# Optimization experiments

Hardware: AMD Instinct MI355X
Metric: run time of the kernel (lower is better)

## Reference

```python
import jax, jax.numpy as jnp
import numpy as np

B, N, D_IN = 32, 4096, 768
D_SLOT, K = 256, 8
D_SHAPE, D_TEX = 128, 128
NUM_ITERS = 3
EPS = 1e-8
LN_EPS = 1e-5


def _ln(x, g, b):
    m = jnp.mean(x, axis=-1, keepdims=True)
    v = jnp.mean((x - m) ** 2, axis=-1, keepdims=True)
    return (x - m) * jax.lax.rsqrt(v + LN_EPS) * g + b


def setup_inputs() -> dict:
    key = jax.random.key(0)
    ks = jax.random.split(key, 20)
    s = lambda fan_in: 1.0 / np.sqrt(fan_in)
    d = {}
    d['features'] = jax.random.normal(ks[0], (B, N, D_IN), dtype=jnp.float32)
    # slot init MLP: d_input -> 2*d_slot -> K*d_slot
    d['Wi1'] = jax.random.uniform(ks[1], (D_IN, 2 * D_SLOT), minval=-s(D_IN), maxval=s(D_IN))
    d['bi1'] = jnp.zeros((2 * D_SLOT,), jnp.float32)
    d['Wi2'] = jax.random.uniform(ks[2], (2 * D_SLOT, K * D_SLOT), minval=-s(2 * D_SLOT), maxval=s(2 * D_SLOT))
    d['bi2'] = jnp.zeros((K * D_SLOT,), jnp.float32)
    # input_proj Linear + LayerNorm
    d['Wp'] = jax.random.uniform(ks[3], (D_IN, D_SLOT), minval=-s(D_IN), maxval=s(D_IN))
    d['bp'] = jnp.zeros((D_SLOT,), jnp.float32)
    d['ln_in_g'] = jnp.ones((D_SLOT,), jnp.float32)
    d['ln_in_b'] = jnp.zeros((D_SLOT,), jnp.float32)
    # attention projections (no bias)
    d['Wqs'] = jax.random.uniform(ks[4], (D_SHAPE, D_SHAPE), minval=-s(D_SHAPE), maxval=s(D_SHAPE))
    d['Wks'] = jax.random.uniform(ks[5], (D_SHAPE, D_SHAPE), minval=-s(D_SHAPE), maxval=s(D_SHAPE))
    d['Wqt'] = jax.random.uniform(ks[6], (D_TEX, D_TEX), minval=-s(D_TEX), maxval=s(D_TEX))
    d['Wkt'] = jax.random.uniform(ks[7], (D_TEX, D_TEX), minval=-s(D_TEX), maxval=s(D_TEX))
    # GRUCell (PyTorch layout, gate order r,z,n), stored as [in, 3*hidden]
    d['W_ih'] = jax.random.uniform(ks[8], (D_SLOT, 3 * D_SLOT), minval=-s(D_SLOT), maxval=s(D_SLOT))
    d['W_hh'] = jax.random.uniform(ks[9], (D_SLOT, 3 * D_SLOT), minval=-s(D_SLOT), maxval=s(D_SLOT))
    d['b_ih'] = jax.random.uniform(ks[10], (3 * D_SLOT,), minval=-s(D_SLOT), maxval=s(D_SLOT))
    d['b_hh'] = jax.random.uniform(ks[11], (3 * D_SLOT,), minval=-s(D_SLOT), maxval=s(D_SLOT))
    # slot LayerNorm + MLP
    d['ln_g'] = jnp.ones((D_SLOT,), jnp.float32)
    d['ln_b'] = jnp.zeros((D_SLOT,), jnp.float32)
    d['Wm1'] = jax.random.uniform(ks[12], (D_SLOT, 2 * D_SLOT), minval=-s(D_SLOT), maxval=s(D_SLOT))
    d['bm1'] = jnp.zeros((2 * D_SLOT,), jnp.float32)
    d['Wm2'] = jax.random.uniform(ks[13], (2 * D_SLOT, D_SLOT), minval=-s(2 * D_SLOT), maxval=s(2 * D_SLOT))
    d['bm2'] = jnp.zeros((D_SLOT,), jnp.float32)
    return d


def _gru(x, h, W_ih, W_hh, b_ih, b_hh):
    gx = x @ W_ih + b_ih  # [M, 3H]
    gh = h @ W_hh + b_hh
    xr, xz, xn = jnp.split(gx, 3, axis=-1)
    hr, hz, hn = jnp.split(gh, 3, axis=-1)
    r = jax.nn.sigmoid(xr + hr)
    z = jax.nn.sigmoid(xz + hz)
    n = jnp.tanh(xn + r * hn)
    return (1.0 - z) * n + z * h


def reference(features, Wi1, bi1, Wi2, bi2, Wp, bp, ln_in_g, ln_in_b,
              Wqs, Wks, Wqt, Wkt, W_ih, W_hh, b_ih, b_hh,
              ln_g, ln_b, Wm1, bm1, Wm2, bm2):
    gelu = lambda x: jax.nn.gelu(x, approximate=False)
    Bsz = features.shape[0]
    # input projection + LN: [B, N, D_SLOT]
    inputs = _ln(features @ Wp + bp, ln_in_g, ln_in_b)
    # probabilistic slot init (eval mode: deterministic branch only)
    feat_pool = jnp.mean(features, axis=1)  # [B, D_IN]
    slots = (gelu(feat_pool @ Wi1 + bi1) @ Wi2 + bi2).reshape(Bsz, K, D_SLOT)
    inp_s = inputs[:, :, :D_SHAPE]
    inp_t = inputs[:, :, D_SHAPE:]
    k_s = inp_s @ Wks  # [B, N, Ds]
    k_t = inp_t @ Wkt
    scale_s = D_SHAPE ** -0.5
    scale_t = D_TEX ** -0.5
    attn = None
    for _ in range(NUM_ITERS):
        q_s = slots[:, :, :D_SHAPE] @ Wqs  # [B, K, Ds]
        q_t = slots[:, :, D_SHAPE:] @ Wqt
        attn_shape = jnp.einsum('bkd,bnd->bkn', q_s, k_s) * scale_s
        attn_tex = jnp.einsum('bkd,bnd->bkn', q_t, k_t) * scale_t
        logits = 0.7 * attn_shape + 0.3 * attn_tex  # [B, K, N]
        attn = jax.nn.softmax(logits, axis=1)  # softmax over slots
        attn_normed = attn / (jnp.sum(attn, axis=-1, keepdims=True) + EPS)
        updates = jnp.einsum('bkn,bnd->bkd', attn_normed, inputs)
        h = _gru(updates.reshape(Bsz * K, D_SLOT), slots.reshape(Bsz * K, D_SLOT),
                 W_ih, W_hh, b_ih, b_hh).reshape(Bsz, K, D_SLOT)
        sn = _ln(h, ln_g, ln_b)
        slots = h + (gelu(sn @ Wm1 + bm1) @ Wm2 + bm2)
    return slots, attn, slots[:, :, :D_SHAPE], slots[:, :, D_SHAPE:]
```

## Files before the change

### kernel.cpp

```cpp
#include <hip/hip_runtime.h>
#include <math.h>

#define NB 32
#define NN 4096
#define DIN 768
#define DS 256
#define KS 8
#define MROWS (NB*NN)

typedef short s8v __attribute__((ext_vector_type(8)));
typedef float f4v __attribute__((ext_vector_type(4)));

__device__ __forceinline__ short f2bf(float f) {
    unsigned u = __builtin_bit_cast(unsigned, f);
    u = (u + 0x7FFFu + ((u >> 16) & 1u)) >> 16;
    return (short)u;
}
__device__ __forceinline__ float bf2f(short s) {
    unsigned u = ((unsigned)(unsigned short)s) << 16;
    return __builtin_bit_cast(float, u);
}
__device__ __forceinline__ float gelu_exact(float x) {
    return 0.5f * x * (1.0f + erff(x * 0.70710678118654752f));
}

__global__ __launch_bounds__(256) void prep_weights(const float* Wp, const float* Wks,
                                                    const float* Wkt, short* Wp_sw, short* Wk_sw) {
    int t = blockIdx.x * 256 + threadIdx.x;
    if (t < 24 * 16 * 64) {
        int s = t / (16 * 64), nt = (t / 64) % 16, l = t % 64;
        int q = l >> 4, m = l & 15;
        #pragma unroll
        for (int j = 0; j < 8; ++j)
            Wp_sw[t * 8 + j] = f2bf(Wp[(s * 32 + q * 8 + j) * 256 + nt * 16 + m]);
    } else if (t < 24 * 16 * 64 + 2 * 4 * 8 * 64) {
        int t2 = t - 24 * 16 * 64;
        int half = t2 / (4 * 8 * 64);
        int r = t2 % (4 * 8 * 64);
        int s = r / (8 * 64), nt = (r / 64) % 8, l = r % 64;
        int q = l >> 4, m = l & 15;
        const float* W = half ? Wkt : Wks;
// ... 138 lines not shown
__global__ __launch_bounds__(256) void k_gemm(const short* inputs_bf, const short* Wk_sw,
                                              short* ksb, short* ktb) {
    int tid = threadIdx.x;
    int wave = tid >> 6, lane = tid & 63, q = lane >> 4, m = lane & 15;
    long rowblk = (long)blockIdx.x * 64;
    long arow = rowblk + wave * 16 + m;
    #pragma unroll
    for (int half = 0; half < 2; ++half) {
        f4v acc[8];
        #pragma unroll
        for (int i = 0; i < 8; ++i) acc[i] = (f4v){0, 0, 0, 0};
        const short* wkh = Wk_sw + half * 16384;
        #pragma unroll
        for (int s4 = 0; s4 < 4; ++s4) {
            s8v a = *(const s8v*)(inputs_bf + arow * 256 + half * 128 + s4 * 32 + q * 8);
            #pragma unroll
            for (int nt = 0; nt < 8; ++nt) {
                s8v bf = *(const s8v*)(wkh + ((s4 * 8 + nt) * 64 + lane) * 8);
                acc[nt] = __builtin_amdgcn_mfma_f32_16x16x32_bf16(a, bf, acc[nt], 0, 0, 0);
            }
        }
        short* out = half ? ktb : ksb;
        #pragma unroll
        for (int nt = 0; nt < 8; ++nt)
            #pragma unroll
            for (int r = 0; r < 4; ++r) {
                long grow = rowblk + wave * 16 + q * 4 + r;
                out[grow * 128 + nt * 16 + m] = f2bf(acc[nt][r]);
            }
    }
}

__global__ __launch_bounds__(256) void q_proj(const float* slots, const float* Wqs,
                                              const float* Wqt, float* qs, float* qt, float* S) {
    __shared__ float sl[1024];
    int b = blockIdx.x, half = blockIdx.y, t = threadIdx.x;
    if (half == 0 && t < 8) S[b * 8 + t] = 0.0f;
    for (int i = 0; i < 4; ++i) {
        int idx = i * 256 + t;
        int k = idx >> 7, d = idx & 127;
        sl[idx] = slots[(b * 8 + k) * 256 + half * 128 + d];
    }
    __syncthreads();
    const float* W = half ? Wqt : Wqs;
    float* out = half ? qt : qs;
    int d = t & 127;
    int k0 = (t >> 7) * 4;
    for (int k = k0; k < k0 + 4; ++k) {
        float acc = 0;
        for (int j = 0; j < 128; ++j) acc += sl[k * 128 + j] * W[j * 128 + d];
        out[(b * 8 + k) * 128 + d] = acc;
    }
}

__global__ __launch_bounds__(256) void attn_kernel(const short* ksb, const short* ktb,
                                                   const float* qs, const float* qt,
                                                   float* attn, float* S) {
    __shared__ float qls[1024], qlt[1024];
    __shared__ float red[32];
    int ntile = blockIdx.x, b = blockIdx.y, t = threadIdx.x;
    for (int i = 0; i < 4; ++i) {
        int idx = i * 256 + t;
        qls[idx] = qs[b * 1024 + idx];
        qlt[idx] = qt[b * 1024 + idx];
    }
    __syncthreads();
    long n = (long)b * 4096 + ntile * 256 + t;
    const short* krs = ksb + n * 128;
    const short* krt = ktb + n * 128;
    float accs[8] = {0, 0, 0, 0, 0, 0, 0, 0};
    float acct[8] = {0, 0, 0, 0, 0, 0, 0, 0};
    for (int c = 0; c < 16; ++c) {
        s8v vs = *(const s8v*)(krs + c * 8);
        s8v vt = *(const s8v*)(krt + c * 8);
        float fs[8], ft[8];
        #pragma unroll
        for (int j = 0; j < 8; ++j) { fs[j] = bf2f(vs[j]); ft[j] = bf2f(vt[j]); }
        #pragma unroll
        for (int k = 0; k < 8; ++k) {
            float as = 0, at = 0;
            #pragma unroll
            for (int j = 0; j < 8; ++j) {
                as += qls[k * 128 + c * 8 + j] * fs[j];
                at += qlt[k * 128 + c * 8 + j] * ft[j];
            }
            accs[k] += as; acct[k] += at;
        }
    }
    const float cs = 0.7f * 0.08838834764831845f;
    const float ct = 0.3f * 0.08838834764831845f;
    float lg[8];
    float mx = -1e30f;
    #pragma unroll
    for (int k = 0; k < 8; ++k) { lg[k] = accs[k] * cs + acct[k] * ct; mx = fmaxf(mx, lg[k]); }
    float se = 0;
    #pragma unroll
    for (int k = 0; k < 8; ++k) { lg[k] = expf(lg[k] - mx); se += lg[k]; }
    float inv = 1.0f / se;
    int nn = ntile * 256 + t;
    #pragma unroll
    for (int k = 0; k < 8; ++k) {
        float a = lg[k] * inv;
        attn[((long)(b * 8 + k)) * 4096 + nn] = a;
        lg[k] = a;
    }
    int lane = t & 63, wv = t >> 6;
    #pragma unroll
    for (int k = 0; k < 8; ++k) {
        float v = lg[k];
        #pragma unroll
        for (int off = 1; off < 64; off <<= 1) v += __shfl_xor(v, off, 64);
        if (lane == 0) red[wv * 8 + k] = v;
    }
    __syncthreads();
    if (t < 8) {
        float s = red[t] + red[8 + t] + red[16 + t] + red[24 + t];
        atomicAdd(&S[b * 8 + t], s);
    }
}

__global__ __launch_bounds__(256) void updates_kernel(const short* inputs_bf, const float* attn,
                                                      const float* S, float* upart) {
    __shared__ unsigned inls[64 * 32];
    __shared__ float atls[8 * 64];
    int bid = blockIdx.x;
    int b = bid >> 4, dt = (bid >> 2) & 3, nq = bid & 3;
    int t = threadIdx.x;
    int k = t >> 5, dp = t & 31;
    float rk = 1.0f / (S[b * 8 + k] + 1e-8f);
    float a0 = 0, a1 = 0;
    for (int ch = 0; ch < 16; ++ch) {
        long n0 = nq * 1024 + ch * 64;
        #pragma unroll
        for (int p = 0; p < 2; ++p) {
            int idx = p * 256 + t;
            int rr = idx >> 3, cc = idx & 7;
            *(uint4*)&inls[rr * 32 + cc * 4] =
                *(const uint4*)(inputs_bf + ((long)b * 4096 + n0 + rr) * 256 + dt * 64 + cc * 8);
        }
        {
            int c2 = (t & 31) * 2;
            float2 av = *(const float2*)(attn + ((long)(b * 8 + k)) * 4096 + n0 + c2);
            atls[k * 64 + c2] = av.x * rk;
            atls[k * 64 + c2 + 1] = av.y * rk;
        }
        __syncthreads();
        #pragma unroll
        for (int j = 0; j < 64; ++j) {
            float a = atls[k * 64 + j];
            unsigned u = inls[j * 32 + dp];
            a0 += a * bf2f((short)(u & 0xFFFF));
            a1 += a * bf2f((short)(u >> 16));
        }
        __syncthreads();
    }
    int bk = b * 8 + k;
    upart[((nq * 256 + bk) * 256) + dt * 64 + dp * 2] = a0;
    upart[((nq * 256 + bk) * 256) + dt * 64 + dp * 2 + 1] = a1;
}

__global__ __launch_bounds__(256) void gru_kernel(const float* upart, const float* W_ih,
                                                  const float* W_hh, const float* b_ih,
                                                  const float* b_hh, const float* ln_g,
                                                  const float* ln_b, const float* Wm1,
                                                  const float* bm1, const float* Wm2,
                                                  const float* bm2, float* slots) {
    __shared__ float u[256], h[256], sn[256], hid[512];
    __shared__ float redA[4], redB[4];
    int bk = blockIdx.x, t = threadIdx.x;
    u[t] = upart[(0 * 256 + bk) * 256 + t] + upart[(1 * 256 + bk) * 256 + t] +
           upart[(2 * 256 + bk) * 256 + t] + upart[(3 * 256 + bk) * 256 + t];
    h[t] = slots[bk * 256 + t];
    __syncthreads();
    float xr = b_ih[t], xz = b_ih[256 + t], xn = b_ih[512 + t];
    float hr = b_hh[t], hz = b_hh[256 + t], hn = b_hh[512 + t];
    for (int j = 0; j < 256; ++j) {
        float uj = u[j], hj = h[j];
        const float* wi = W_ih + j * 768 + t;
        const float* wh = W_hh + j * 768 + t;
        xr += uj * wi[0]; xz += uj * wi[256]; xn += uj * wi[512];
        hr += hj * wh[0]; hz += hj * wh[256]; hn += hj * wh[512];
    }
    float rg = 1.0f / (1.0f + expf(-(xr + hr)));
    float zg = 1.0f / (1.0f + expf(-(xz + hz)));
    float ng = tanhf(xn + rg * hn);
    float hnew = (1.0f - zg) * ng + zg * h[t];
    float v1 = hnew, v2 = hnew * hnew;
    int lane = t & 63, wv = t >> 6;
    #pragma unroll
    for (int off = 1; off < 64; off <<= 1) {
        v1 += __shfl_xor(v1, off, 64);
        v2 += __shfl_xor(v2, off, 64);
    }
    if (lane == 0) { redA[wv] = v1; redB[wv] = v2; }
    __syncthreads();
    float sm = redA[0] + redA[1] + redA[2] + redA[3];
    float sq = redB[0] + redB[1] + redB[2] + redB[3];
    float mean = sm * (1.0f / 256.0f);
    float var = sq * (1.0f / 256.0f) - mean * mean;
    float rstd = rsqrtf(var + 1e-5f);
    sn[t] = (hnew - mean) * rstd * ln_g[t] + ln_b[t];
    __syncthreads();
    float m1 = bm1[t], m2 = bm1[256 + t];
    for (int j = 0; j < 256; ++j) {
        float s = sn[j];
        m1 += s * Wm1[j * 512 + t];
        m2 += s * Wm1[j * 512 + 256 + t];
    }
    hid[t] = gelu_exact(m1);
    hid[256 + t] = gelu_exact(m2);
    __syncthreads();
    float o = bm2[t];
    for (int j = 0; j < 512; ++j) o += hid[j] * Wm2[j * 256 + t];
    slots[bk * 256 + t] = hnew + o;
}

__global__ __launch_bounds__(256) void pack_out(const float* slots, const float* attn,
                                                float* out) {
    long i = (long)blockIdx.x * 256 + threadIdx.x;
    if (i >= 1179648) return;
    float v;
    if (i < 65536) v = slots[i];
    else if (i < 1114112) v = attn[i - 65536];
    else {
        long j = i - 1114112;
        if (j < 32768) v = slots[(j >> 7) * 256 + (j & 127)];
        else { long j2 = j - 32768; v = slots[(j2 >> 7) * 256 + 128 + (j2 & 127)]; }
    }
    out[i] = v;
}

extern "C" void kernel_launch(void* const* d_in, const int* in_sizes, int n_in,
                              void* d_out, int out_size, void* d_ws, size_t ws_size,
                              hipStream_t stream) {
    const float* feat    = (const float*)d_in[0];
    const float* Wi1     = (const float*)d_in[1];
    const float* bi1     = (const float*)d_in[2];
    const float* Wi2     = (const float*)d_in[3];
    const float* bi2     = (const float*)d_in[4];
    const float* Wp      = (const float*)d_in[5];
    const float* bp      = (const float*)d_in[6];
    const float* ln_in_g = (const float*)d_in[7];
    const float* ln_in_b = (const float*)d_in[8];
    const float* Wqs     = (const float*)d_in[9];
    const float* Wks     = (const float*)d_in[10];
    const float* Wqt     = (const float*)d_in[11];
    const float* Wkt     = (const float*)d_in[12];
    const float* W_ih    = (const float*)d_in[13];
    const float* W_hh    = (const float*)d_in[14];
    const float* b_ih    = (const float*)d_in[15];
    const float* b_hh    = (const float*)d_in[16];
    const float* ln_g    = (const float*)d_in[17];
    const float* ln_b    = (const float*)d_in[18];
    const float* Wm1     = (const float*)d_in[19];
    const float* bm1     = (const float*)d_in[20];
    const float* Wm2     = (const float*)d_in[21];
    const float* bm2     = (const float*)d_in[22];
    float* out = (float*)d_out;

    char* ws = (char*)d_ws;
    short* inputs_bf = (short*)ws; ws += 67108864;
    short* ksb       = (short*)ws; ws += 33554432;
    short* ktb       = (short*)ws; ws += 33554432;
    float* attn      = (float*)ws; ws += 4194304;
    float* slots     = (float*)ws; ws += 262144;
    float* qsb       = (float*)ws; ws += 131072;
    float* qtb       = (float*)ws; ws += 131072;
    float* ppart     = (float*)ws; ws += 3145728;
    short* Wp_sw     = (short*)ws; ws += 393216;
    short* Wk_sw     = (short*)ws; ws += 65536;
    float* hidb      = (float*)ws; ws += 65536;
    float* S         = (float*)ws; ws += 1024;
    float* upart     = (float*)ws; ws += 1048576;

    prep_weights<<<112, 256, 0, stream>>>(Wp, Wks, Wkt, Wp_sw, Wk_sw);
    gemm_in_ln<<<1024, 256, 0, stream>>>(feat, Wp_sw, bp, ln_in_g, ln_in_b, inputs_bf, ppart);
    slots_hid<<<dim3(32, 2), 256, 0, stream>>>(ppart, Wi1, bi1, hidb);
    slots_out<<<256, 256, 0, stream>>>(hidb, Wi2, bi2, slots);
    k_gemm<<<2048, 256, 0, stream>>>(inputs_bf, Wk_sw, ksb, ktb);
    for (int it = 0; it < 3; ++it) {
        q_proj<<<dim3(32, 2), 256, 0, stream>>>(slots, Wqs, Wqt, qsb, qtb, S);
        attn_kernel<<<dim3(16, 32), 256, 0, stream>>>(ksb, ktb, qsb, qtb, attn, S);
        updates_kernel<<<512, 256, 0, stream>>>(inputs_bf, attn, S, upart);
        gru_kernel<<<256, 256, 0, stream>>>(upart, W_ih, W_hh, b_ih, b_hh, ln_g, ln_b,
                                            Wm1, bm1, Wm2, bm2, slots);
    }
    pack_out<<<4608, 256, 0, stream>>>(slots, attn, out);
}
```

Baseline: 1.109 ms.

## Batch four slot rows per GRU block and widen update tiles to halve input reloads

The GRU/MLP kernel now processes four slot rows per block, so each weight element loaded from global memory is reused across four rows instead of one, and the grid shrinks from 256 to 64 blocks. The updates kernel now covers 128 feature columns per block instead of 64, so each thread accumulates four outputs and the attention tile is loaded half as often. Both changes cut redundant global loads. The cost is lower parallelism (64 and 256 blocks on a large GPU) and more registers and shared memory per block.

```diff
diff --git a/kernel.cpp b/kernel.cpp
--- a/kernel.cpp
+++ b/kernel.cpp
@@ -300,42 +300,44 @@
 
 __global__ __launch_bounds__(256) void updates_kernel(const short* inputs_bf, const float* attn,
                                                       const float* S, float* upart) {
-    __shared__ unsigned inls[64 * 32];
+    __shared__ unsigned inls[64 * 64];
     __shared__ float atls[8 * 64];
     int bid = blockIdx.x;
-    int b = bid >> 4, dt = (bid >> 2) & 3, nq = bid & 3;
+    int b = bid >> 3, dth = (bid >> 2) & 1, nq = bid & 3;
     int t = threadIdx.x;
     int k = t >> 5, dp = t & 31;
     float rk = 1.0f / (S[b * 8 + k] + 1e-8f);
-    float a0 = 0, a1 = 0;
+    float a0 = 0, a1 = 0, a2 = 0, a3 = 0;
     for (int ch = 0; ch < 16; ++ch) {
-        long n0 = nq * 1024 + ch * 64;
-        #pragma unroll
-        for (int p = 0; p < 2; ++p) {
+        long n0 = (long)nq * 1024 + ch * 64;
+        #pragma unroll
+        for (int p = 0; p < 4; ++p) {
             int idx = p * 256 + t;
-            int rr = idx >> 3, cc = idx & 7;
-            *(uint4*)&inls[rr * 32 + cc * 4] =
-                *(const uint4*)(inputs_bf + ((long)b * 4096 + n0 + rr) * 256 + dt * 64 + cc * 8);
+            int rr = idx >> 4, cc = idx & 15;
+            *(uint4*)&inls[rr * 64 + cc * 4] =
+                *(const uint4*)(inputs_bf + ((long)b * 4096 + n0 + rr) * 256 + dth * 128 + cc * 8);
         }
         {
-            int c2 = (t & 31) * 2;
+            int c2 = dp * 2;
             float2 av = *(const float2*)(attn + ((long)(b * 8 + k)) * 4096 + n0 + c2);
             atls[k * 64 + c2] = av.x * rk;
             atls[k * 64 + c2 + 1] = av.y * rk;
         }
         __syncthreads();
-        #pragma unroll
+        #pragma unroll 16
         for (int j = 0; j < 64; ++j) {
             float a = atls[k * 64 + j];
-            unsigned u = inls[j * 32 + dp];
-            a0 += a * bf2f((short)(u & 0xFFFF));
-            a1 += a * bf2f((short)(u >> 16));
+            uint2 uu = *(const uint2*)&inls[j * 64 + dp * 2];
+            a0 += a * bf2f((short)(uu.x & 0xFFFF));
+            a1 += a * bf2f((short)(uu.x >> 16));
+            a2 += a * bf2f((short)(uu.y & 0xFFFF));
+            a3 += a * bf2f((short)(uu.y >> 16));
         }
         __syncthreads();
     }
     int bk = b * 8 + k;
-    upart[((nq * 256 + bk) * 256) + dt * 64 + dp * 2] = a0;
-    upart[((nq * 256 + bk) * 256) + dt * 64 + dp * 2 + 1] = a1;
+    float* o = upart + ((long)(nq * 256 + bk)) * 256 + dth * 128 + dp * 4;
+    o[0] = a0; o[1] = a1; o[2] = a2; o[3] = a3;
 }
 
 __global__ __launch_bounds__(256) void gru_kernel(const float* upart, const float* W_ih,
@@ -344,54 +346,94 @@
                                                   const float* ln_b, const float* Wm1,
                                                   const float* bm1, const float* Wm2,
                                                   const float* bm2, float* slots) {
-    __shared__ float u[256], h[256], sn[256], hid[512];
-    __shared__ float redA[4], redB[4];
-    int bk = blockIdx.x, t = threadIdx.x;
-    u[t] = upart[(0 * 256 + bk) * 256 + t] + upart[(1 * 256 + bk) * 256 + t] +
-           upart[(2 * 256 + bk) * 256 + t] + upart[(3 * 256 + bk) * 256 + t];
-    h[t] = slots[bk * 256 + t];
-    __syncthreads();
-    float xr = b_ih[t], xz = b_ih[256 + t], xn = b_ih[512 + t];
-    float hr = b_hh[t], hz = b_hh[256 + t], hn = b_hh[512 + t];
+    __shared__ float u[4][256], h[4][256], sn[4][256], hid[4][512];
+    __shared__ float redA[4][4], redB[4][4];
+    int bk0 = blockIdx.x * 4, t = threadIdx.x;
+    #pragma unroll
+    for (int r = 0; r < 4; ++r) {
+        int bk = bk0 + r;
+        u[r][t] = upart[(0 * 256 + bk) * 256 + t] + upart[(1 * 256 + bk) * 256 + t] +
+                  upart[(2 * 256 + bk) * 256 + t] + upart[(3 * 256 + bk) * 256 + t];
+        h[r][t] = slots[bk * 256 + t];
+    }
+    __syncthreads();
+    float bir = b_ih[t], biz = b_ih[256 + t], bin_ = b_ih[512 + t];
+    float bhr = b_hh[t], bhz = b_hh[256 + t], bhn = b_hh[512 + t];
+    float xr[4], xz[4], xn[4], hr[4], hz[4], hn[4];
+    #pragma unroll
+    for (int r = 0; r < 4; ++r) {
+        xr[r] = bir; xz[r] = biz; xn[r] = bin_;
+        hr[r] = bhr; hz[r] = bhz; hn[r] = bhn;
+    }
+    #pragma unroll 2
     for (int j = 0; j < 256; ++j) {
-        float uj = u[j], hj = h[j];
-        const float* wi = W_ih + j * 768 + t;
-        const float* wh = W_hh + j * 768 + t;
-        xr += uj * wi[0]; xz += uj * wi[256]; xn += uj * wi[512];
-        hr += hj * wh[0]; hz += hj * wh[256]; hn += hj * wh[512];
-    }
-    float rg = 1.0f / (1.0f + expf(-(xr + hr)));
-    float zg = 1.0f / (1.0f + expf(-(xz + hz)));
-    float ng = tanhf(xn + rg * hn);
-    float hnew = (1.0f - zg) * ng + zg * h[t];
-    float v1 = hnew, v2 = hnew * hnew;
+        float wir = W_ih[j * 768 + t], wiz = W_ih[j * 768 + 256 + t], win = W_ih[j * 768 + 512 + t];
+        float whr = W_hh[j * 768 + t], whz = W_hh[j * 768 + 256 + t], whn = W_hh[j * 768 + 512 + t];
+        #pragma unroll
+        for (int r = 0; r < 4; ++r) {
+            float uj = u[r][j], hj = h[r][j];
+            xr[r] += uj * wir; xz[r] += uj * wiz; xn[r] += uj * win;
+            hr[r] += hj * whr; hz[r] += hj * whz; hn[r] += hj * whn;
+        }
+    }
+    float hnew[4];
     int lane = t & 63, wv = t >> 6;
     #pragma unroll
-    for (int off = 1; off < 64; off <<= 1) {
-        v1 += __shfl_xor(v1, off, 64);
-        v2 += __shfl_xor(v2, off, 64);
-    }
-    if (lane == 0) { redA[wv] = v1; redB[wv] = v2; }
-    __syncthreads();
-    float sm = redA[0] + redA[1] + redA[2] + redA[3];
-    float sq = redB[0] + redB[1] + redB[2] + redB[3];
-    float mean = sm * (1.0f / 256.0f);
-    float var = sq * (1.0f / 256.0f) - mean * mean;
-    float rstd = rsqrtf(var + 1e-5f);
-    sn[t] = (hnew - mean) * rstd * ln_g[t] + ln_b[t];
-    __syncthreads();
-    float m1 = bm1[t], m2 = bm1[256 + t];
+    for (int r = 0; r < 4; ++r) {
+        float rg = 1.0f / (1.0f + expf(-(xr[r] + hr[r])));
+        float zg = 1.0f / (1.0f + expf(-(xz[r] + hz[r])));
+        float ng = tanhf(xn[r] + rg * hn[r]);
+        hnew[r] = (1.0f - zg) * ng + zg * h[r][t];
+        float v1 = hnew[r], v2 = hnew[r] * hnew[r];
+        #pragma unroll
+        for (int off = 1; off < 64; off <<= 1) {
+            v1 += __shfl_xor(v1, off, 64);
+            v2 += __shfl_xor(v2, off, 64);
+        }
+        if (lane == 0) { redA[r][wv] = v1; redB[r][wv] = v2; }
+    }
+    __syncthreads();
+    #pragma unroll
+    for (int r = 0; r < 4; ++r) {
+        float sm = redA[r][0] + redA[r][1] + redA[r][2] + redA[r][3];
+        float sq = redB[r][0] + redB[r][1] + redB[r][2] + redB[r][3];
+        float mean = sm * (1.0f / 256.0f);
+        float var = sq * (1.0f / 256.0f) - mean * mean;
+        float rstd = rsqrtf(var + 1e-5f);
+        sn[r][t] = (hnew[r] - mean) * rstd * ln_g[t] + ln_b[t];
+    }
+    __syncthreads();
+    float m1[4], m2[4];
+    float b1 = bm1[t], b2 = bm1[256 + t];
+    #pragma unroll
+    for (int r = 0; r < 4; ++r) { m1[r] = b1; m2[r] = b2; }
+    #pragma unroll 2
     for (int j = 0; j < 256; ++j) {
-        float s = sn[j];
-        m1 += s * Wm1[j * 512 + t];
-        m2 += s * Wm1[j * 512 + 256 + t];
-    }
-    hid[t] = gelu_exact(m1);
-    hid[256 + t] = gelu_exact(m2);
-    __syncthreads();
-    float o = bm2[t];
-    for (int j = 0; j < 512; ++j) o += hid[j] * Wm2[j * 256 + t];
-    slots[bk * 256 + t] = hnew + o;
+        float w1 = Wm1[j * 512 + t], w2 = Wm1[j * 512 + 256 + t];
+        #pragma unroll
+        for (int r = 0; r < 4; ++r) {
+            float s = sn[r][j];
+            m1[r] += s * w1; m2[r] += s * w2;
+        }
+    }
+    #pragma unroll
+    for (int r = 0; r < 4; ++r) {
+        hid[r][t] = gelu_exact(m1[r]);
+        hid[r][256 + t] = gelu_exact(m2[r]);
+    }
+    __syncthreads();
+    float o[4];
+    float bo = bm2[t];
+    #pragma unroll
+    for (int r = 0; r < 4; ++r) o[r] = bo;
+    #pragma unroll 2
+    for (int j = 0; j < 512; ++j) {
+        float w = Wm2[j * 256 + t];
+        #pragma unroll
+        for (int r = 0; r < 4; ++r) o[r] += hid[r][j] * w;
+    }
+    #pragma unroll
+    for (int r = 0; r < 4; ++r) slots[(bk0 + r) * 256 + t] = hnew[r] + o[r];
 }
 
 __global__ __launch_bounds__(256) void pack_out(const float* slots, const float* attn,
@@ -460,9 +502,9 @@
     for (int it = 0; it < 3; ++it) {
         q_proj<<<dim3(32, 2), 256, 0, stream>>>(slots, Wqs, Wqt, qsb, qtb, S);
         attn_kernel<<<dim3(16, 32), 256, 0, stream>>>(ksb, ktb, qsb, qtb, attn, S);
-        updates_kernel<<<512, 256, 0, stream>>>(inputs_bf, attn, S, upart);
-        gru_kernel<<<256, 256, 0, stream>>>(upart, W_ih, W_hh, b_ih, b_hh, ln_g, ln_b,
-                                            Wm1, bm1, Wm2, bm2, slots);
+        updates_kernel<<<256, 256, 0, stream>>>(inputs_bf, attn, S, upart);
+        gru_kernel<<<64, 256, 0, stream>>>(upart, W_ih, W_hh, b_ih, b_hh, ln_g, ln_b,
+                                           Wm1, bm1, Wm2, bm2, slots);
     }
     pack_out<<<4608, 256, 0, stream>>>(slots, attn, out);
 }
```

New measurement: 1.492 ms. +34.6%, slower.

## Fuse slot-attention iterations into one persistent cooperative kernel with grid syncs

Applied to the files above, without the earlier changes.

Replaces the per-iteration q_proj/attn/updates/GRU launches and the final pack kernel with a single cooperative kernel of 256 blocks × 512 threads that uses grid.sync between phases. Attention is written straight into the output buffer. The atomic slot-sum becomes per-tile partial sums that the update phase reduces, and the next iteration's query projection is folded into the GRU phase. This removes about 13 kernel launches and their gaps, but the GRU phase leaves half of each block idle, and grid-wide barriers plus a fixed 256-block grid may limit occupancy in the memory-heavy phases.

```diff
diff --git a/kernel.cpp b/kernel.cpp
--- a/kernel.cpp
+++ b/kernel.cpp
@@ -1,12 +1,14 @@
 #include <hip/hip_runtime.h>
+#include <hip/hip_cooperative_groups.h>
 #include <math.h>
+
+namespace cg = cooperative_groups;
 
 #define NB 32
 #define NN 4096
 #define DIN 768
 #define DS 256
 #define KS 8
-#define MROWS (NB*NN)
 
 typedef short s8v __attribute__((ext_vector_type(8)));
 typedef float f4v __attribute__((ext_vector_type(4)));
@@ -211,10 +213,9 @@
 }
 
 __global__ __launch_bounds__(256) void q_proj(const float* slots, const float* Wqs,
-                                              const float* Wqt, float* qs, float* qt, float* S) {
+                                              const float* Wqt, float* qs, float* qt) {
     __shared__ float sl[1024];
     int b = blockIdx.x, half = blockIdx.y, t = threadIdx.x;
-    if (half == 0 && t < 8) S[b * 8 + t] = 0.0f;
     for (int i = 0; i < 4; ++i) {
         int idx = i * 256 + t;
         int k = idx >> 7, d = idx & 127;
@@ -232,181 +233,207 @@
     }
 }
 
-__global__ __launch_bounds__(256) void attn_kernel(const short* ksb, const short* ktb,
-                                                   const float* qs, const float* qt,
-                                                   float* attn, float* S) {
-    __shared__ float qls[1024], qlt[1024];
-    __shared__ float red[32];
-    int ntile = blockIdx.x, b = blockIdx.y, t = threadIdx.x;
-    for (int i = 0; i < 4; ++i) {
-        int idx = i * 256 + t;
-        qls[idx] = qs[b * 1024 + idx];
-        qlt[idx] = qt[b * 1024 + idx];
-    }
-    __syncthreads();
-    long n = (long)b * 4096 + ntile * 256 + t;
-    const short* krs = ksb + n * 128;
-    const short* krt = ktb + n * 128;
-    float accs[8] = {0, 0, 0, 0, 0, 0, 0, 0};
-    float acct[8] = {0, 0, 0, 0, 0, 0, 0, 0};
-    for (int c = 0; c < 16; ++c) {
-        s8v vs = *(const s8v*)(krs + c * 8);
-        s8v vt = *(const s8v*)(krt + c * 8);
-        float fs[8], ft[8];
-        #pragma unroll
-        for (int j = 0; j < 8; ++j) { fs[j] = bf2f(vs[j]); ft[j] = bf2f(vt[j]); }
-        #pragma unroll
-        for (int k = 0; k < 8; ++k) {
-            float as = 0, at = 0;
-            #pragma unroll
-            for (int j = 0; j < 8; ++j) {
-                as += qls[k * 128 + c * 8 + j] * fs[j];
-                at += qlt[k * 128 + c * 8 + j] * ft[j];
-            }
-            accs[k] += as; acct[k] += at;
-        }
-    }
-    const float cs = 0.7f * 0.08838834764831845f;
-    const float ct = 0.3f * 0.08838834764831845f;
-    float lg[8];
-    float mx = -1e30f;
-    #pragma unroll
-    for (int k = 0; k < 8; ++k) { lg[k] = accs[k] * cs + acct[k] * ct; mx = fmaxf(mx, lg[k]); }
-    float se = 0;
-    #pragma unroll
-    for (int k = 0; k < 8; ++k) { lg[k] = expf(lg[k] - mx); se += lg[k]; }
-    float inv = 1.0f / se;
-    int nn = ntile * 256 + t;
-    #pragma unroll
-    for (int k = 0; k < 8; ++k) {
-        float a = lg[k] * inv;
-        attn[((long)(b * 8 + k)) * 4096 + nn] = a;
-        lg[k] = a;
-    }
+struct AttnS { float qls[1024]; float qlt[1024]; float red[2][32]; };
+struct UpdS  { unsigned inls[2][2048]; float atls[2][512]; };
+struct GruS  { float u[256], h[256], sn[256], hid[512], redA[4], redB[4]; };
+
+__global__ __launch_bounds__(512, 2) void iter_kernel(
+    const short* ksb, const short* ktb, const short* inputs_bf,
+    float* qs, float* qt, float* attn, float* Spart, float* upart, float* slots,
+    const float* W_ih, const float* W_hh, const float* b_ih, const float* b_hh,
+    const float* ln_g, const float* ln_b, const float* Wm1, const float* bm1,
+    const float* Wm2, const float* bm2, const float* Wqs, const float* Wqt,
+    float* out) {
+    cg::grid_group grid = cg::this_grid();
+    __shared__ union { AttnS a; UpdS up; GruS g; } sh;
+    int bid = blockIdx.x;
+    int tid = threadIdx.x;
+    int half = tid >> 8;
+    int t = tid & 255;
     int lane = t & 63, wv = t >> 6;
-    #pragma unroll
-    for (int k = 0; k < 8; ++k) {
-        float v = lg[k];
-        #pragma unroll
-        for (int off = 1; off < 64; off <<= 1) v += __shfl_xor(v, off, 64);
-        if (lane == 0) red[wv * 8 + k] = v;
-    }
-    __syncthreads();
-    if (t < 8) {
-        float s = red[t] + red[8 + t] + red[16 + t] + red[24 + t];
-        atomicAdd(&S[b * 8 + t], s);
-    }
-}
-
-__global__ __launch_bounds__(256) void updates_kernel(const short* inputs_bf, const float* attn,
-                                                      const float* S, float* upart) {
-    __shared__ unsigned inls[64 * 32];
-    __shared__ float atls[8 * 64];
-    int bid = blockIdx.x;
-    int b = bid >> 4, dt = (bid >> 2) & 3, nq = bid & 3;
-    int t = threadIdx.x;
-    int k = t >> 5, dp = t & 31;
-    float rk = 1.0f / (S[b * 8 + k] + 1e-8f);
-    float a0 = 0, a1 = 0;
-    for (int ch = 0; ch < 16; ++ch) {
-        long n0 = nq * 1024 + ch * 64;
-        #pragma unroll
-        for (int p = 0; p < 2; ++p) {
-            int idx = p * 256 + t;
-            int rr = idx >> 3, cc = idx & 7;
-            *(uint4*)&inls[rr * 32 + cc * 4] =
-                *(const uint4*)(inputs_bf + ((long)b * 4096 + n0 + rr) * 256 + dt * 64 + cc * 8);
-        }
+
+    for (int it = 0; it < 3; ++it) {
         {
-            int c2 = (t & 31) * 2;
-            float2 av = *(const float2*)(attn + ((long)(b * 8 + k)) * 4096 + n0 + c2);
-            atls[k * 64 + c2] = av.x * rk;
-            atls[k * 64 + c2 + 1] = av.y * rk;
-        }
-        __syncthreads();
-        #pragma unroll
-        for (int j = 0; j < 64; ++j) {
-            float a = atls[k * 64 + j];
-            unsigned u = inls[j * 32 + dp];
-            a0 += a * bf2f((short)(u & 0xFFFF));
-            a1 += a * bf2f((short)(u >> 16));
-        }
-        __syncthreads();
-    }
-    int bk = b * 8 + k;
-    upart[((nq * 256 + bk) * 256) + dt * 64 + dp * 2] = a0;
-    upart[((nq * 256 + bk) * 256) + dt * 64 + dp * 2 + 1] = a1;
-}
-
-__global__ __launch_bounds__(256) void gru_kernel(const float* upart, const float* W_ih,
-                                                  const float* W_hh, const float* b_ih,
-                                                  const float* b_hh, const float* ln_g,
-                                                  const float* ln_b, const float* Wm1,
-                                                  const float* bm1, const float* Wm2,
-                                                  const float* bm2, float* slots) {
-    __shared__ float u[256], h[256], sn[256], hid[512];
-    __shared__ float redA[4], redB[4];
-    int bk = blockIdx.x, t = threadIdx.x;
-    u[t] = upart[(0 * 256 + bk) * 256 + t] + upart[(1 * 256 + bk) * 256 + t] +
-           upart[(2 * 256 + bk) * 256 + t] + upart[(3 * 256 + bk) * 256 + t];
-    h[t] = slots[bk * 256 + t];
-    __syncthreads();
-    float xr = b_ih[t], xz = b_ih[256 + t], xn = b_ih[512 + t];
-    float hr = b_hh[t], hz = b_hh[256 + t], hn = b_hh[512 + t];
-    for (int j = 0; j < 256; ++j) {
-        float uj = u[j], hj = h[j];
-        const float* wi = W_ih + j * 768 + t;
-        const float* wh = W_hh + j * 768 + t;
-        xr += uj * wi[0]; xz += uj * wi[256]; xn += uj * wi[512];
-        hr += hj * wh[0]; hz += hj * wh[256]; hn += hj * wh[512];
-    }
-    float rg = 1.0f / (1.0f + expf(-(xr + hr)));
-    float zg = 1.0f / (1.0f + expf(-(xz + hz)));
-    float ng = tanhf(xn + rg * hn);
-    float hnew = (1.0f - zg) * ng + zg * h[t];
-    float v1 = hnew, v2 = hnew * hnew;
-    int lane = t & 63, wv = t >> 6;
-    #pragma unroll
-    for (int off = 1; off < 64; off <<= 1) {
-        v1 += __shfl_xor(v1, off, 64);
-        v2 += __shfl_xor(v2, off, 64);
-    }
-    if (lane == 0) { redA[wv] = v1; redB[wv] = v2; }
-    __syncthreads();
-    float sm = redA[0] + redA[1] + redA[2] + redA[3];
-    float sq = redB[0] + redB[1] + redB[2] + redB[3];
-    float mean = sm * (1.0f / 256.0f);
-    float var = sq * (1.0f / 256.0f) - mean * mean;
-    float rstd = rsqrtf(var + 1e-5f);
-    sn[t] = (hnew - mean) * rstd * ln_g[t] + ln_b[t];
-    __syncthreads();
-    float m1 = bm1[t], m2 = bm1[256 + t];
-    for (int j = 0; j < 256; ++j) {
-        float s = sn[j];
-        m1 += s * Wm1[j * 512 + t];
-        m2 += s * Wm1[j * 512 + 256 + t];
-    }
-    hid[t] = gelu_exact(m1);
-    hid[256 + t] = gelu_exact(m2);
-    __syncthreads();
-    float o = bm2[t];
-    for (int j = 0; j < 512; ++j) o += hid[j] * Wm2[j * 256 + t];
-    slots[bk * 256 + t] = hnew + o;
-}
-
-__global__ __launch_bounds__(256) void pack_out(const float* slots, const float* attn,
-                                                float* out) {
-    long i = (long)blockIdx.x * 256 + threadIdx.x;
-    if (i >= 1179648) return;
-    float v;
-    if (i < 65536) v = slots[i];
-    else if (i < 1114112) v = attn[i - 65536];
-    else {
-        long j = i - 1114112;
-        if (j < 32768) v = slots[(j >> 7) * 256 + (j & 127)];
-        else { long j2 = j - 32768; v = slots[(j2 >> 7) * 256 + 128 + (j2 & 127)]; }
-    }
-    out[i] = v;
+            int b = bid >> 3;
+            int ntile = ((bid & 7) << 1) | half;
+            #pragma unroll
+            for (int i = 0; i < 2; ++i) {
+                int idx = i * 512 + tid;
+                sh.a.qls[idx] = qs[b * 1024 + idx];
+                sh.a.qlt[idx] = qt[b * 1024 + idx];
+            }
+            __syncthreads();
+            long n = (long)b * 4096 + ntile * 256 + t;
+            const short* krs = ksb + n * 128;
+            const short* krt = ktb + n * 128;
+            float accs[8] = {0, 0, 0, 0, 0, 0, 0, 0};
+            float acct[8] = {0, 0, 0, 0, 0, 0, 0, 0};
+            for (int c = 0; c < 16; ++c) {
+                s8v vs = *(const s8v*)(krs + c * 8);
+                s8v vt = *(const s8v*)(krt + c * 8);
+                float fs[8], ft[8];
+                #pragma unroll
+                for (int j = 0; j < 8; ++j) { fs[j] = bf2f(vs[j]); ft[j] = bf2f(vt[j]); }
+                #pragma unroll
+                for (int k = 0; k < 8; ++k) {
+                    float as = 0, at = 0;
+                    #pragma unroll
+                    for (int j = 0; j < 8; ++j) {
+                        as += sh.a.qls[k * 128 + c * 8 + j] * fs[j];
+                        at += sh.a.qlt[k * 128 + c * 8 + j] * ft[j];
+                    }
+                    accs[k] += as; acct[k] += at;
+                }
+            }
+            const float cs = 0.7f * 0.08838834764831845f;
+            const float ct = 0.3f * 0.08838834764831845f;
+            float lg[8];
+            float mx = -1e30f;
+            #pragma unroll
+            for (int k = 0; k < 8; ++k) { lg[k] = accs[k] * cs + acct[k] * ct; mx = fmaxf(mx, lg[k]); }
+            float se = 0;
+            #pragma unroll
+            for (int k = 0; k < 8; ++k) { lg[k] = expf(lg[k] - mx); se += lg[k]; }
+            float inv = 1.0f / se;
+            int nn = ntile * 256 + t;
+            #pragma unroll
+            for (int k = 0; k < 8; ++k) {
+                float a = lg[k] * inv;
+                attn[((long)(b * 8 + k)) * 4096 + nn] = a;
+                lg[k] = a;
+            }
+            #pragma unroll
+            for (int k = 0; k < 8; ++k) {
+                float v = lg[k];
+                #pragma unroll
+                for (int off = 1; off < 64; off <<= 1) v += __shfl_xor(v, off, 64);
+                if (lane == 0) sh.a.red[half][wv * 8 + k] = v;
+            }
+            __syncthreads();
+            if (t < 8) {
+                float s = sh.a.red[half][t] + sh.a.red[half][8 + t] +
+                          sh.a.red[half][16 + t] + sh.a.red[half][24 + t];
+                Spart[(b * 8 + t) * 16 + ntile] = s;
+            }
+        }
+        grid.sync();
+        {
+            int u = half * 256 + bid;
+            int b = u >> 4, dt = (u >> 2) & 3, nq = u & 3;
+            int k = t >> 5, dp = t & 31;
+            const float* spp = Spart + (b * 8 + k) * 16;
+            float sp = 0;
+            #pragma unroll
+            for (int i = 0; i < 16; ++i) sp += spp[i];
+            float rk = 1.0f / (sp + 1e-8f);
+            unsigned* inls = sh.up.inls[half];
+            float* atls = sh.up.atls[half];
+            float a0 = 0, a1 = 0;
+            for (int ch = 0; ch < 16; ++ch) {
+                long n0 = nq * 1024 + ch * 64;
+                #pragma unroll
+                for (int p = 0; p < 2; ++p) {
+                    int idx = p * 256 + t;
+                    int rr = idx >> 3, cc = idx & 7;
+                    *(uint4*)&inls[rr * 32 + cc * 4] =
+                        *(const uint4*)(inputs_bf + ((long)b * 4096 + n0 + rr) * 256 + dt * 64 + cc * 8);
+                }
+                {
+                    int c2 = (t & 31) * 2;
+                    float2 av = *(const float2*)(attn + ((long)(b * 8 + k)) * 4096 + n0 + c2);
+                    atls[k * 64 + c2] = av.x * rk;
+                    atls[k * 64 + c2 + 1] = av.y * rk;
+                }
+                __syncthreads();
+                #pragma unroll
+                for (int j = 0; j < 64; ++j) {
+                    float a = atls[k * 64 + j];
+                    unsigned uu = inls[j * 32 + dp];
+                    a0 += a * bf2f((short)(uu & 0xFFFF));
+                    a1 += a * bf2f((short)(uu >> 16));
+                }
+                __syncthreads();
+            }
+            int bk = b * 8 + k;
+            upart[((nq * 256 + bk) * 256) + dt * 64 + dp * 2] = a0;
+            upart[((nq * 256 + bk) * 256) + dt * 64 + dp * 2 + 1] = a1;
+        }
+        grid.sync();
+        {
+            int bk = bid;
+            if (half == 0) {
+                sh.g.u[t] = upart[(0 * 256 + bk) * 256 + t] + upart[(1 * 256 + bk) * 256 + t] +
+                            upart[(2 * 256 + bk) * 256 + t] + upart[(3 * 256 + bk) * 256 + t];
+                sh.g.h[t] = slots[bk * 256 + t];
+            }
+            __syncthreads();
+            float hnew = 0.0f;
+            if (half == 0) {
+                float xr = b_ih[t], xz = b_ih[256 + t], xn = b_ih[512 + t];
+                float hr = b_hh[t], hz = b_hh[256 + t], hn = b_hh[512 + t];
+                for (int j = 0; j < 256; ++j) {
+                    float uj = sh.g.u[j], hj = sh.g.h[j];
+                    const float* wi = W_ih + j * 768 + t;
+                    const float* wh = W_hh + j * 768 + t;
+                    xr += uj * wi[0]; xz += uj * wi[256]; xn += uj * wi[512];
+                    hr += hj * wh[0]; hz += hj * wh[256]; hn += hj * wh[512];
+                }
+                float rg = 1.0f / (1.0f + expf(-(xr + hr)));
+                float zg = 1.0f / (1.0f + expf(-(xz + hz)));
+                float ng = tanhf(xn + rg * hn);
+                hnew = (1.0f - zg) * ng + zg * sh.g.h[t];
+                float v1 = hnew, v2 = hnew * hnew;
+                #pragma unroll
+                for (int off = 1; off < 64; off <<= 1) {
+                    v1 += __shfl_xor(v1, off, 64);
+                    v2 += __shfl_xor(v2, off, 64);
+                }
+                if (lane == 0) { sh.g.redA[wv] = v1; sh.g.redB[wv] = v2; }
+            }
+            __syncthreads();
+            if (half == 0) {
+                float sm = sh.g.redA[0] + sh.g.redA[1] + sh.g.redA[2] + sh.g.redA[3];
+                float sq = sh.g.redB[0] + sh.g.redB[1] + sh.g.redB[2] + sh.g.redB[3];
+                float mean = sm * (1.0f / 256.0f);
+                float var = sq * (1.0f / 256.0f) - mean * mean;
+                float rstd = rsqrtf(var + 1e-5f);
+                sh.g.sn[t] = (hnew - mean) * rstd * ln_g[t] + ln_b[t];
+            }
+            __syncthreads();
+            if (half == 0) {
+                float m1 = bm1[t], m2 = bm1[256 + t];
+                for (int j = 0; j < 256; ++j) {
+                    float s = sh.g.sn[j];
+                    m1 += s * Wm1[j * 512 + t];
+                    m2 += s * Wm1[j * 512 + 256 + t];
+                }
+                sh.g.hid[t] = gelu_exact(m1);
+                sh.g.hid[256 + t] = gelu_exact(m2);
+            }
+            __syncthreads();
+            if (half == 0) {
+                float o = bm2[t];
+                for (int j = 0; j < 512; ++j) o += sh.g.hid[j] * Wm2[j * 256 + t];
+                float v = hnew + o;
+                slots[bk * 256 + t] = v;
+                if (it == 2) {
+                    out[bk * 256 + t] = v;
+                    if (t < 128) out[1114112 + bk * 128 + t] = v;
+                    else out[1114112 + 32768 + bk * 128 + (t - 128)] = v;
+                }
+                sh.g.u[t] = v;
+            }
+            __syncthreads();
+            if (half == 0 && it != 2) {
+                int qh = t >> 7, d = t & 127;
+                const float* W = qh ? Wqt : Wqs;
+                float qa = 0;
+                for (int j = 0; j < 128; ++j) qa += sh.g.u[qh * 128 + j] * W[j * 128 + d];
+                (qh ? qt : qs)[bk * 128 + d] = qa;
+            }
+        }
+        grid.sync();
+    }
 }
 
 extern "C" void kernel_launch(void* const* d_in, const int* in_sizes, int n_in,
@@ -436,12 +463,13 @@
     const float* Wm2     = (const float*)d_in[21];
     const float* bm2     = (const float*)d_in[22];
     float* out = (float*)d_out;
+    float* outAttn = out + 65536;
 
     char* ws = (char*)d_ws;
     short* inputs_bf = (short*)ws; ws += 67108864;
     short* ksb       = (short*)ws; ws += 33554432;
     short* ktb       = (short*)ws; ws += 33554432;
-    float* attn      = (float*)ws; ws += 4194304;
+    ws += 4194304;
     float* slots     = (float*)ws; ws += 262144;
     float* qsb       = (float*)ws; ws += 131072;
     float* qtb       = (float*)ws; ws += 131072;
@@ -449,7 +477,7 @@
     short* Wp_sw     = (short*)ws; ws += 393216;
     short* Wk_sw     = (short*)ws; ws += 65536;
     float* hidb      = (float*)ws; ws += 65536;
-    float* S         = (float*)ws; ws += 1024;
+    float* Spart     = (float*)ws; ws += 16384;
     float* upart     = (float*)ws; ws += 1048576;
 
     prep_weights<<<112, 256, 0, stream>>>(Wp, Wks, Wkt, Wp_sw, Wk_sw);
@@ -457,12 +485,17 @@
     slots_hid<<<dim3(32, 2), 256, 0, stream>>>(ppart, Wi1, bi1, hidb);
     slots_out<<<256, 256, 0, stream>>>(hidb, Wi2, bi2, slots);
     k_gemm<<<2048, 256, 0, stream>>>(inputs_bf, Wk_sw, ksb, ktb);
-    for (int it = 0; it < 3; ++it) {
-        q_proj<<<dim3(32, 2), 256, 0, stream>>>(slots, Wqs, Wqt, qsb, qtb, S);
-        attn_kernel<<<dim3(16, 32), 256, 0, stream>>>(ksb, ktb, qsb, qtb, attn, S);
-        updates_kernel<<<512, 256, 0, stream>>>(inputs_bf, attn, S, upart);
-        gru_kernel<<<256, 256, 0, stream>>>(upart, W_ih, W_hh, b_ih, b_hh, ln_g, ln_b,
-                                            Wm1, bm1, Wm2, bm2, slots);
-    }
-    pack_out<<<4608, 256, 0, stream>>>(slots, attn, out);
-}
+    q_proj<<<dim3(32, 2), 256, 0, stream>>>(slots, Wqs, Wqt, qsb, qtb);
+    {
+        void* kargs[] = {
+            (void*)&ksb, (void*)&ktb, (void*)&inputs_bf,
+            (void*)&qsb, (void*)&qtb, (void*)&outAttn, (void*)&Spart, (void*)&upart,
+            (void*)&slots,
+            (void*)&W_ih, (void*)&W_hh, (void*)&b_ih, (void*)&b_hh,
+            (void*)&ln_g, (void*)&ln_b, (void*)&Wm1, (void*)&bm1,
+            (void*)&Wm2, (void*)&bm2, (void*)&Wqs, (void*)&Wqt,
+            (void*)&out};
+        hipLaunchCooperativeKernel((const void*)iter_kernel, dim3(256), dim3(512),
+                                   kargs, 0, stream);
+    }
+}
```

New measurement: 1.391 ms. +25.4%, slower.

## Fuse attention with update accumulation and fold q-projection and output packing into GRU

Applied to the files above, without the earlier changes.

Merges the attention/softmax kernel with the weighted-update reduction so attention weights stay in shared memory instead of round-tripping through global memory. The per-slot normalisation sum is written as per-tile partials rather than atomics, and the GRU kernel now reduces 16 partials and applies the 1/S scaling. The next iteration's query projection and the final output writes also move into the GRU kernel, which removes the separate q_proj (after the first) and pack_out launches. In exchange the upart partial buffer grows 16x and each att_upd block loops over all four feature quarters serially.

```diff
diff --git a/kernel.cpp b/kernel.cpp
--- a/kernel.cpp
+++ b/kernel.cpp
@@ -6,7 +6,6 @@
 #define DIN 768
 #define DS 256
 #define KS 8
-#define MROWS (NB*NN)
 
 typedef short s8v __attribute__((ext_vector_type(8)));
 typedef float f4v __attribute__((ext_vector_type(4)));
@@ -211,10 +210,9 @@
 }
 
 __global__ __launch_bounds__(256) void q_proj(const float* slots, const float* Wqs,
-                                              const float* Wqt, float* qs, float* qt, float* S) {
+                                              const float* Wqt, float* qs, float* qt) {
     __shared__ float sl[1024];
     int b = blockIdx.x, half = blockIdx.y, t = threadIdx.x;
-    if (half == 0 && t < 8) S[b * 8 + t] = 0.0f;
     for (int i = 0; i < 4; ++i) {
         int idx = i * 256 + t;
         int k = idx >> 7, d = idx & 127;
@@ -232,123 +230,129 @@
     }
 }
 
-__global__ __launch_bounds__(256) void attn_kernel(const short* ksb, const short* ktb,
-                                                   const float* qs, const float* qt,
-                                                   float* attn, float* S) {
-    __shared__ float qls[1024], qlt[1024];
+__global__ __launch_bounds__(256) void att_upd(const short* ksb, const short* ktb,
+                                               const short* inputs_bf,
+                                               const float* qs, const float* qt,
+                                               float* attnOut, float* Spart, float* upart,
+                                               int final_it) {
+    __shared__ union { float q[2048]; unsigned inls[2048]; } shq;
+    __shared__ float atls[2048];
     __shared__ float red[32];
     int ntile = blockIdx.x, b = blockIdx.y, t = threadIdx.x;
+    int lane = t & 63, wv = t >> 6;
+    #pragma unroll
     for (int i = 0; i < 4; ++i) {
         int idx = i * 256 + t;
-        qls[idx] = qs[b * 1024 + idx];
-        qlt[idx] = qt[b * 1024 + idx];
-    }
-    __syncthreads();
-    long n = (long)b * 4096 + ntile * 256 + t;
-    const short* krs = ksb + n * 128;
-    const short* krt = ktb + n * 128;
-    float accs[8] = {0, 0, 0, 0, 0, 0, 0, 0};
-    float acct[8] = {0, 0, 0, 0, 0, 0, 0, 0};
-    for (int c = 0; c < 16; ++c) {
-        s8v vs = *(const s8v*)(krs + c * 8);
-        s8v vt = *(const s8v*)(krt + c * 8);
-        float fs[8], ft[8];
-        #pragma unroll
-        for (int j = 0; j < 8; ++j) { fs[j] = bf2f(vs[j]); ft[j] = bf2f(vt[j]); }
+        shq.q[idx] = qs[b * 1024 + idx];
+        shq.q[1024 + idx] = qt[b * 1024 + idx];
+    }
+    __syncthreads();
+    {
+        long n = (long)b * 4096 + ntile * 256 + t;
+        const short* krs = ksb + n * 128;
+        const short* krt = ktb + n * 128;
+        float accs[8] = {0, 0, 0, 0, 0, 0, 0, 0};
+        float acct[8] = {0, 0, 0, 0, 0, 0, 0, 0};
+        for (int c = 0; c < 16; ++c) {
+            s8v vs = *(const s8v*)(krs + c * 8);
+            s8v vt = *(const s8v*)(krt + c * 8);
+            float fs[8], ft[8];
+            #pragma unroll
+            for (int j = 0; j < 8; ++j) { fs[j] = bf2f(vs[j]); ft[j] = bf2f(vt[j]); }
+            #pragma unroll
+            for (int k = 0; k < 8; ++k) {
+                float as = 0, at = 0;
+                #pragma unroll
+                for (int j = 0; j < 8; ++j) {
+                    as += shq.q[k * 128 + c * 8 + j] * fs[j];
+                    at += shq.q[1024 + k * 128 + c * 8 + j] * ft[j];
+                }
+                accs[k] += as; acct[k] += at;
+            }
+        }
+        const float cs = 0.7f * 0.08838834764831845f;
+        const float ct = 0.3f * 0.08838834764831845f;
+        float lg[8];
+        float mx = -1e30f;
+        #pragma unroll
+        for (int k = 0; k < 8; ++k) { lg[k] = accs[k] * cs + acct[k] * ct; mx = fmaxf(mx, lg[k]); }
+        float se = 0;
+        #pragma unroll
+        for (int k = 0; k < 8; ++k) { lg[k] = expf(lg[k] - mx); se += lg[k]; }
+        float inv = 1.0f / se;
+        int nn = ntile * 256 + t;
         #pragma unroll
         for (int k = 0; k < 8; ++k) {
-            float as = 0, at = 0;
-            #pragma unroll
-            for (int j = 0; j < 8; ++j) {
-                as += qls[k * 128 + c * 8 + j] * fs[j];
-                at += qlt[k * 128 + c * 8 + j] * ft[j];
-            }
-            accs[k] += as; acct[k] += at;
-        }
-    }
-    const float cs = 0.7f * 0.08838834764831845f;
-    const float ct = 0.3f * 0.08838834764831845f;
-    float lg[8];
-    float mx = -1e30f;
-    #pragma unroll
-    for (int k = 0; k < 8; ++k) { lg[k] = accs[k] * cs + acct[k] * ct; mx = fmaxf(mx, lg[k]); }
-    float se = 0;
-    #pragma unroll
-    for (int k = 0; k < 8; ++k) { lg[k] = expf(lg[k] - mx); se += lg[k]; }
-    float inv = 1.0f / se;
-    int nn = ntile * 256 + t;
-    #pragma unroll
-    for (int k = 0; k < 8; ++k) {
-        float a = lg[k] * inv;
-        attn[((long)(b * 8 + k)) * 4096 + nn] = a;
-        lg[k] = a;
-    }
-    int lane = t & 63, wv = t >> 6;
-    #pragma unroll
-    for (int k = 0; k < 8; ++k) {
-        float v = lg[k];
-        #pragma unroll
-        for (int off = 1; off < 64; off <<= 1) v += __shfl_xor(v, off, 64);
-        if (lane == 0) red[wv * 8 + k] = v;
-    }
-    __syncthreads();
-    if (t < 8) {
-        float s = red[t] + red[8 + t] + red[16 + t] + red[24 + t];
-        atomicAdd(&S[b * 8 + t], s);
-    }
-}
-
-__global__ __launch_bounds__(256) void updates_kernel(const short* inputs_bf, const float* attn,
-                                                      const float* S, float* upart) {
-    __shared__ unsigned inls[64 * 32];
-    __shared__ float atls[8 * 64];
-    int bid = blockIdx.x;
-    int b = bid >> 4, dt = (bid >> 2) & 3, nq = bid & 3;
-    int t = threadIdx.x;
+            float a = lg[k] * inv;
+            atls[k * 256 + t] = a;
+            if (final_it) attnOut[((long)(b * 8 + k)) * 4096 + nn] = a;
+            lg[k] = a;
+        }
+        #pragma unroll
+        for (int k = 0; k < 8; ++k) {
+            float v = lg[k];
+            #pragma unroll
+            for (int off = 1; off < 64; off <<= 1) v += __shfl_xor(v, off, 64);
+            if (lane == 0) red[wv * 8 + k] = v;
+        }
+        __syncthreads();
+        if (t < 8) {
+            float s = red[t] + red[8 + t] + red[16 + t] + red[24 + t];
+            Spart[(b * 8 + t) * 16 + ntile] = s;
+        }
+    }
     int k = t >> 5, dp = t & 31;
-    float rk = 1.0f / (S[b * 8 + k] + 1e-8f);
-    float a0 = 0, a1 = 0;
-    for (int ch = 0; ch < 16; ++ch) {
-        long n0 = nq * 1024 + ch * 64;
-        #pragma unroll
-        for (int p = 0; p < 2; ++p) {
-            int idx = p * 256 + t;
-            int rr = idx >> 3, cc = idx & 7;
-            *(uint4*)&inls[rr * 32 + cc * 4] =
-                *(const uint4*)(inputs_bf + ((long)b * 4096 + n0 + rr) * 256 + dt * 64 + cc * 8);
-        }
-        {
-            int c2 = (t & 31) * 2;
-            float2 av = *(const float2*)(attn + ((long)(b * 8 + k)) * 4096 + n0 + c2);
-            atls[k * 64 + c2] = av.x * rk;
-            atls[k * 64 + c2 + 1] = av.y * rk;
-        }
-        __syncthreads();
-        #pragma unroll
-        for (int j = 0; j < 64; ++j) {
-            float a = atls[k * 64 + j];
-            unsigned u = inls[j * 32 + dp];
-            a0 += a * bf2f((short)(u & 0xFFFF));
-            a1 += a * bf2f((short)(u >> 16));
-        }
-        __syncthreads();
-    }
     int bk = b * 8 + k;
-    upart[((nq * 256 + bk) * 256) + dt * 64 + dp * 2] = a0;
-    upart[((nq * 256 + bk) * 256) + dt * 64 + dp * 2 + 1] = a1;
-}
-
-__global__ __launch_bounds__(256) void gru_kernel(const float* upart, const float* W_ih,
-                                                  const float* W_hh, const float* b_ih,
-                                                  const float* b_hh, const float* ln_g,
-                                                  const float* ln_b, const float* Wm1,
-                                                  const float* bm1, const float* Wm2,
-                                                  const float* bm2, float* slots) {
+    for (int dt = 0; dt < 4; ++dt) {
+        float a0 = 0, a1 = 0;
+        for (int ch = 0; ch < 4; ++ch) {
+            #pragma unroll
+            for (int p = 0; p < 2; ++p) {
+                int idx = p * 256 + t;
+                int rr = idx >> 3, cc = idx & 7;
+                *(uint4*)&shq.inls[rr * 32 + cc * 4] =
+                    *(const uint4*)(inputs_bf +
+                                    ((long)b * 4096 + ntile * 256 + ch * 64 + rr) * 256 +
+                                    dt * 64 + cc * 8);
+            }
+            __syncthreads();
+            #pragma unroll
+            for (int j = 0; j < 64; ++j) {
+                float a = atls[k * 256 + ch * 64 + j];
+                unsigned uu = shq.inls[j * 32 + dp];
+                a0 += a * bf2f((short)(uu & 0xFFFF));
+                a1 += a * bf2f((short)(uu >> 16));
+            }
+            __syncthreads();
+        }
+        upart[((long)(ntile * 256 + bk)) * 256 + dt * 64 + dp * 2] = a0;
+        upart[((long)(ntile * 256 + bk)) * 256 + dt * 64 + dp * 2 + 1] = a1;
+    }
+}
+
+__global__ __launch_bounds__(256) void gru_kernel(const float* upart, const float* Spart,
+                                                  const float* W_ih, const float* W_hh,
+                                                  const float* b_ih, const float* b_hh,
+                                                  const float* ln_g, const float* ln_b,
+                                                  const float* Wm1, const float* bm1,
+                                                  const float* Wm2, const float* bm2,
+                                                  float* slots, const float* Wqs,
+                                                  const float* Wqt, float* qs, float* qt,
+                                                  float* out, int final_it) {
     __shared__ float u[256], h[256], sn[256], hid[512];
     __shared__ float redA[4], redB[4];
     int bk = blockIdx.x, t = threadIdx.x;
-    u[t] = upart[(0 * 256 + bk) * 256 + t] + upart[(1 * 256 + bk) * 256 + t] +
-           upart[(2 * 256 + bk) * 256 + t] + upart[(3 * 256 + bk) * 256 + t];
+    {
+        const float* spp = Spart + bk * 16;
+        float S = 0;
+        #pragma unroll
+        for (int i = 0; i < 16; ++i) S += spp[i];
+        float rS = 1.0f / (S + 1e-8f);
+        float us = 0;
+        #pragma unroll
+        for (int nq = 0; nq < 16; ++nq) us += upart[((long)(nq * 256 + bk)) * 256 + t];
+        u[t] = us * rS;
+    }
     h[t] = slots[bk * 256 + t];
     __syncthreads();
     float xr = b_ih[t], xz = b_ih[256 + t], xn = b_ih[512 + t];
@@ -391,22 +395,21 @@
     __syncthreads();
     float o = bm2[t];
     for (int j = 0; j < 512; ++j) o += hid[j] * Wm2[j * 256 + t];
-    slots[bk * 256 + t] = hnew + o;
-}
-
-__global__ __launch_bounds__(256) void pack_out(const float* slots, const float* attn,
-                                                float* out) {
-    long i = (long)blockIdx.x * 256 + threadIdx.x;
-    if (i >= 1179648) return;
-    float v;
-    if (i < 65536) v = slots[i];
-    else if (i < 1114112) v = attn[i - 65536];
-    else {
-        long j = i - 1114112;
-        if (j < 32768) v = slots[(j >> 7) * 256 + (j & 127)];
-        else { long j2 = j - 32768; v = slots[(j2 >> 7) * 256 + 128 + (j2 & 127)]; }
-    }
-    out[i] = v;
+    float v = hnew + o;
+    slots[bk * 256 + t] = v;
+    if (!final_it) {
+        u[t] = v;
+        __syncthreads();
+        int half = t >> 7, d = t & 127;
+        const float* W = half ? Wqt : Wqs;
+        float qa = 0;
+        for (int j = 0; j < 128; ++j) qa += u[half * 128 + j] * W[j * 128 + d];
+        (half ? qt : qs)[bk * 128 + d] = qa;
+    } else {
+        out[bk * 256 + t] = v;
+        if (t < 128) out[1114112 + bk * 128 + t] = v;
+        else out[1114112 + 32768 + bk * 128 + (t - 128)] = v;
+    }
 }
 
 extern "C" void kernel_launch(void* const* d_in, const int* in_sizes, int n_in,
@@ -436,12 +439,12 @@
     const float* Wm2     = (const float*)d_in[21];
     const float* bm2     = (const float*)d_in[22];
     float* out = (float*)d_out;
+    float* outAttn = out + 65536;
 
     char* ws = (char*)d_ws;
     short* inputs_bf = (short*)ws; ws += 67108864;
     short* ksb       = (short*)ws; ws += 33554432;
     short* ktb       = (short*)ws; ws += 33554432;
-    float* attn      = (float*)ws; ws += 4194304;
     float* slots     = (float*)ws; ws += 262144;
     float* qsb       = (float*)ws; ws += 131072;
     float* qtb       = (float*)ws; ws += 131072;
@@ -449,20 +452,20 @@
     short* Wp_sw     = (short*)ws; ws += 393216;
     short* Wk_sw     = (short*)ws; ws += 65536;
     float* hidb      = (float*)ws; ws += 65536;
-    float* S         = (float*)ws; ws += 1024;
-    float* upart     = (float*)ws; ws += 1048576;
+    float* Spart     = (float*)ws; ws += 16384;
+    float* upart     = (float*)ws; ws += 16777216;
 
     prep_weights<<<112, 256, 0, stream>>>(Wp, Wks, Wkt, Wp_sw, Wk_sw);
     gemm_in_ln<<<1024, 256, 0, stream>>>(feat, Wp_sw, bp, ln_in_g, ln_in_b, inputs_bf, ppart);
     slots_hid<<<dim3(32, 2), 256, 0, stream>>>(ppart, Wi1, bi1, hidb);
     slots_out<<<256, 256, 0, stream>>>(hidb, Wi2, bi2, slots);
     k_gemm<<<2048, 256, 0, stream>>>(inputs_bf, Wk_sw, ksb, ktb);
+    q_proj<<<dim3(32, 2), 256, 0, stream>>>(slots, Wqs, Wqt, qsb, qtb);
     for (int it = 0; it < 3; ++it) {
-        q_proj<<<dim3(32, 2), 256, 0, stream>>>(slots, Wqs, Wqt, qsb, qtb, S);
-        attn_kernel<<<dim3(16, 32), 256, 0, stream>>>(ksb, ktb, qsb, qtb, attn, S);
-        updates_kernel<<<512, 256, 0, stream>>>(inputs_bf, attn, S, upart);
-        gru_kernel<<<256, 256, 0, stream>>>(upart, W_ih, W_hh, b_ih, b_hh, ln_g, ln_b,
-                                            Wm1, bm1, Wm2, bm2, slots);
-    }
-    pack_out<<<4608, 256, 0, stream>>>(slots, attn, out);
-}
+        att_upd<<<dim3(16, 32), 256, 0, stream>>>(ksb, ktb, inputs_bf, qsb, qtb,
+                                                  outAttn, Spart, upart, it == 2 ? 1 : 0);
+        gru_kernel<<<256, 256, 0, stream>>>(upart, Spart, W_ih, W_hh, b_ih, b_hh,
+                                            ln_g, ln_b, Wm1, bm1, Wm2, bm2, slots,
+                                            Wqs, Wqt, qsb, qtb, out, it == 2 ? 1 : 0);
+    }
+}
```

After: 1.109 ms. Within noise of the previous version (+0.0%).
